# Performance work log

Hardware: AMD Instinct MI355X
Metric: run time of the kernel (lower is better)

Reference implementation:

```python
import jax, jax.numpy as jnp
import numpy as np

B, C, D, O = 64, 64, 512, 256
N_REG, G = 8, 8  # 8 regions of 8 channels


def setup_inputs() -> dict:
    key = jax.random.key(0)
    ks = jax.random.split(key, 9)
    std = 0.02  # init_weights_classify: normal(0, 0.02) for Linear weights, zero bias
    x = jax.random.normal(ks[0], (B, C, D), dtype=jnp.float32)
    region_indices = jnp.arange(C, dtype=jnp.int32).reshape(N_REG, G)
    # attn_fc: Linear(2D -> D), ReLU, Linear(D -> 1)
    W1 = jax.random.normal(ks[1], (2 * D, D), dtype=jnp.float32) * std
    b1 = jnp.zeros((D,), jnp.float32)
    W2 = jax.random.normal(ks[2], (D, 1), dtype=jnp.float32) * std
    b2 = jnp.zeros((1,), jnp.float32)
    # gcn1: Linear(D -> D); gcn2: Linear(D -> O)
    Wg1 = jax.random.normal(ks[3], (D, D), dtype=jnp.float32) * std
    bg1 = jnp.zeros((D,), jnp.float32)
    Wg2 = jax.random.normal(ks[4], (D, O), dtype=jnp.float32) * std
    bg2 = jnp.zeros((O,), jnp.float32)
    return {"x": x, "W1": W1, "b1": b1, "W2": W2, "b2": b2,
            "Wg1": Wg1, "bg1": bg1, "Wg2": Wg2, "bg2": bg2,
            "region_indices": region_indices}


def _leaky_relu02(z):
    return jnp.where(z >= 0, z, 0.2 * z)


def reference(x, W1, b1, W2, b2, Wg1, bg1, Wg2, bg2, region_indices):
    Bb, Cc, Dd = x.shape
    n_reg, g = region_indices.shape
    # channel -> region id; mask[i,j] = same region and i != j
    rid = jnp.zeros((Cc,), jnp.int32).at[region_indices.reshape(-1)].set(
        jnp.repeat(jnp.arange(n_reg, dtype=jnp.int32), g))
    idx = jnp.arange(Cc)
    mask = (rid[:, None] == rid[None, :]) & (idx[:, None] != idx[None, :])  # [C, C]
    # attn_fc on cat(x_i, x_j): split first linear to avoid [B,C,C,2D] concat
    a = x @ W1[:Dd]   # [B, C, D]
    bpart = x @ W1[Dd:]  # [B, C, D]
    h = jax.nn.relu(a[:, :, None, :] + bpart[:, None, :, :] + b1)  # [B, C, C, D]
    scores = jnp.einsum('bijd,do->bij', h, W2) + b2[0]  # [B, C, C]
    scores = jnp.where(mask[None, :, :], scores, -jnp.inf)
    adj = jax.nn.softmax(scores, axis=-1)  # [B, C, C]
    # gcn1: adj @ x -> Linear -> LeakyReLU(0.2); residual mix
    m1 = jnp.einsum('bij,bjd->bid', adj, x)
    x1 = _leaky_relu02(m1 @ Wg1 + bg1)
    x1 = 0.5 * x1 + 0.5 * x
    # gcn2
    m2 = jnp.einsum('bij,bjd->bid', adj, x1)
    out = _leaky_relu02(m2 @ Wg2 + bg2)  # [B, C, O]
    return out
```

## Files before the change

### kernel.cpp

```cpp
#include <hip/hip_runtime.h>
#include <math.h>

#define B_   64
#define C_   64
#define D_   512
#define O_   256
#define NREG 8
#define G_   8
#define M_   (B_ * C_)

typedef __attribute__((ext_vector_type(8))) short s16x8;
typedef __attribute__((ext_vector_type(4))) float f32x4;
typedef unsigned short u16;
typedef unsigned int   u32;

__device__ __forceinline__ float bf2f(u16 u) {
    u32 v = ((u32)u) << 16;
    return __uint_as_float(v);
}
__device__ __forceinline__ u16 f2bf(float f) {
    u32 u = __float_as_uint(f);
    u32 r = (u + 0x7FFFu + ((u >> 16) & 1u)) >> 16;
    return (u16)r;
}

__global__ void rid_kernel(const int* __restrict__ region_indices, int* __restrict__ rid) {
    int t = threadIdx.x;
    int r = t / G_;
    int ch = region_indices[t];
    rid[ch] = r;
}

__global__ __launch_bounds__(256) void f32_to_bf16_vec(const float* __restrict__ in,
                                                       u16* __restrict__ out, int n8) {
    int i = blockIdx.x * blockDim.x + threadIdx.x;
    if (i >= n8) return;
    const float4* p = (const float4*)(in + (size_t)i * 8);
    float4 v0 = p[0], v1 = p[1];
    s16x8 o;
    o[0] = (short)f2bf(v0.x); o[1] = (short)f2bf(v0.y);
    o[2] = (short)f2bf(v0.z); o[3] = (short)f2bf(v0.w);
    o[4] = (short)f2bf(v1.x); o[5] = (short)f2bf(v1.y);
    o[6] = (short)f2bf(v1.z); o[7] = (short)f2bf(v1.w);
    *(s16x8*)(out + (size_t)i * 8) = o;
}

__global__ __launch_bounds__(256) void transpose_to_bf16(const float* __restrict__ W,
                                                         u16* __restrict__ Wt, int K, int N) {
    __shared__ float tile[32][33];
    int n0 = blockIdx.x * 32, k0 = blockIdx.y * 32;
    int tx = threadIdx.x, ty = threadIdx.y;
    #pragma unroll
    for (int j = 0; j < 4; j++)
        tile[ty + j * 8][tx] = W[(size_t)(k0 + ty + j * 8) * N + n0 + tx];
    __syncthreads();
    #pragma unroll
    for (int j = 0; j < 4; j++)
        Wt[(size_t)(n0 + ty + j * 8) * K + k0 + tx] = f2bf(tile[tx][ty + j * 8]);
}

#define LDP 40

template<int BM, int BN, int EPI>
__global__ __launch_bounds__(256)
void mfma_gemm(const u16* __restrict__ A, const u16* __restrict__ Bt, int ldbt,
               u16* __restrict__ Cbf0, u16* __restrict__ Cbf1,
               const float* __restrict__ bias, const float* __restrict__ resid,
               float* __restrict__ Cf)
{
    constexpr int K   = 512;
    constexpr int MR  = BM / 32;
    constexpr int NR  = BN / 32;
    constexpr int CHA = (BM * 32) / (256 * 8);
    constexpr int CHB = (BN * 32) / (256 * 8);
    constexpr int NBH = 512 / BN;

    __shared__ __align__(16) u16 As[BM][LDP];
    __shared__ __align__(16) u16 Bs[BN][LDP];

    const int tid  = threadIdx.x;
    const int lane = tid & 63, w = tid >> 6;
    const int wr = w >> 1, wc = w & 1;
    const int lr = lane & 15, lq = lane >> 4;

    const int bx = blockIdx.x, by = blockIdx.y;
    const int m0 = by * BM;
    int nbase, koff;
    if (EPI == 0) { nbase = (bx % NBH) * BN; koff = (bx / NBH) * 512; }
    else          { nbase = bx * BN;         koff = 0; }

    const int ar = tid >> 2;
    const int ac = (tid & 3) * 8;

    f32x4 acc[MR][NR] = {};
    s16x8 stA[CHA], stB[CHB];

    auto loadG = [&](int kt) {
        #pragma unroll
        for (int ch = 0; ch < CHA; ch++)
            stA[ch] = *(const s16x8*)(A + (size_t)(m0 + ar + ch * 64) * K + kt + ac);
        #pragma unroll
        for (int ch = 0; ch < CHB; ch++)
            stB[ch] = *(const s16x8*)(Bt + (size_t)(nbase + ar + ch * 64) * ldbt + koff + kt + ac);
    };

    loadG(0);
    for (int kt = 0; kt < K; kt += 32) {
        __syncthreads();
        #pragma unroll
        for (int ch = 0; ch < CHA; ch++)
            *(s16x8*)(&As[ar + ch * 64][ac]) = stA[ch];
        #pragma unroll
        for (int ch = 0; ch < CHB; ch++)
            *(s16x8*)(&Bs[ar + ch * 64][ac]) = stB[ch];
        __syncthreads();
        if (kt + 32 < K) loadG(kt + 32);

        s16x8 af[MR], bfr[NR];
        #pragma unroll
        for (int m = 0; m < MR; m++)
            af[m] = *(const s16x8*)(&As[wr * (BM / 2) + m * 16 + lr][lq * 8]);
        #pragma unroll
        for (int n = 0; n < NR; n++)
            bfr[n] = *(const s16x8*)(&Bs[wc * (BN / 2) + n * 16 + lr][lq * 8]);
        #pragma unroll
        for (int m = 0; m < MR; m++)
            #pragma unroll
            for (int n = 0; n < NR; n++)
                acc[m][n] = __builtin_amdgcn_mfma_f32_16x16x32_bf16(af[m], bfr[n], acc[m][n], 0, 0, 0);
    }

    #pragma unroll
    for (int m = 0; m < MR; m++) {
        #pragma unroll
        for (int n = 0; n < NR; n++) {
            #pragma unroll
            for (int j = 0; j < 4; j++) {
                int row = m0 + wr * (BM / 2) + m * 16 + lq * 4 + j;
                int col = nbase + wc * (BN / 2) + n * 16 + lr;
                float v = acc[m][n][j];
                if (EPI == 0) {
                    u16* dst = koff ? Cbf1 : Cbf0;
                    dst[(size_t)row * 512 + col] = f2bf(v);
                } else if (EPI == 1) {
                    v += bias[col];
                    v = (v >= 0.f) ? v : 0.2f * v;
                    v = 0.5f * v + 0.5f * resid[(size_t)row * 512 + col];
                    Cbf0[(size_t)row * 512 + col] = f2bf(v);
                } else {
                    v += bias[col];
                    v = (v >= 0.f) ? v : 0.2f * v;
                    Cf[(size_t)row * 256 + col] = v;
                }
            }
        }
    }
}

__global__ __launch_bounds__(64)
void scores_m1_kernel(const u16* __restrict__ a, const u16* __restrict__ bpart,
                      const float* __restrict__ x,
                      const float* __restrict__ b1, const float* __restrict__ W2,
                      const float* __restrict__ b2,
                      const int* __restrict__ region_indices, const int* __restrict__ rid,
                      float* __restrict__ adjw, u16* __restrict__ m1)
{
    const int lane = threadIdx.x;
    const int bi = blockIdx.x;
    const int b = bi / C_, i = bi % C_;
    const int r = rid[i];

    int members[G_];
    #pragma unroll
    for (int m = 0; m < G_; m++) members[m] = region_indices[r * G_ + m];

    const int d0 = lane * 8;
    float ai[8], w2v[8];
    s16x8 av8 = *(const s16x8*)(a + (size_t)bi * D_ + d0);
    const float4* b1v = (const float4*)(b1 + d0);
    const float4* w2p = (const float4*)(W2 + d0);
    float4 b1a = b1v[0], b1b = b1v[1];
    float4 w2a = w2p[0], w2b = w2p[1];
    ai[0] = bf2f((u16)av8[0]) + b1a.x; ai[1] = bf2f((u16)av8[1]) + b1a.y;
    ai[2] = bf2f((u16)av8[2]) + b1a.z; ai[3] = bf2f((u16)av8[3]) + b1a.w;
    ai[4] = bf2f((u16)av8[4]) + b1b.x; ai[5] = bf2f((u16)av8[5]) + b1b.y;
    ai[6] = bf2f((u16)av8[6]) + b1b.z; ai[7] = bf2f((u16)av8[7]) + b1b.w;
    w2v[0] = w2a.x; w2v[1] = w2a.y; w2v[2] = w2a.z; w2v[3] = w2a.w;
    w2v[4] = w2b.x; w2v[5] = w2b.y; w2v[6] = w2b.z; w2v[7] = w2b.w;

    const float bias2 = b2[0];
    float sc[G_];
    float scmax = -INFINITY;
    for (int m = 0; m < G_; m++) {
        int j = members[m];
        if (j == i) { sc[m] = -INFINITY; continue; }
        s16x8 bv8 = *(const s16x8*)(bpart + ((size_t)(b * C_ + j)) * D_ + d0);
        float p = 0.f;
        #pragma unroll
        for (int t = 0; t < 8; t++) {
            float h = ai[t] + bf2f((u16)bv8[t]);
            h = (h > 0.f) ? h : 0.f;
            p += h * w2v[t];
        }
        #pragma unroll
        for (int off = 32; off >= 1; off >>= 1) p += __shfl_xor(p, off);
        sc[m] = p + bias2;
        scmax = fmaxf(scmax, sc[m]);
    }

    float esum = 0.f, wgt[G_];
    for (int m = 0; m < G_; m++) {
        if (sc[m] == -INFINITY) { wgt[m] = 0.f; continue; }
        wgt[m] = expf(sc[m] - scmax);
        esum += wgt[m];
    }
    const float inv = 1.f / esum;

    float accv[8] = {};
    for (int m = 0; m < G_; m++) {
        wgt[m] *= inv;
        if (wgt[m] == 0.f) continue;
        int j = members[m];
        const float4* xp = (const float4*)(x + ((size_t)(b * C_ + j)) * D_ + d0);
        float4 xa = xp[0], xb = xp[1];
        accv[0] += wgt[m] * xa.x; accv[1] += wgt[m] * xa.y;
        accv[2] += wgt[m] * xa.z; accv[3] += wgt[m] * xa.w;
        accv[4] += wgt[m] * xb.x; accv[5] += wgt[m] * xb.y;
        accv[6] += wgt[m] * xb.z; accv[7] += wgt[m] * xb.w;
    }
    s16x8 o;
    #pragma unroll
    for (int t = 0; t < 8; t++) o[t] = (short)f2bf(accv[t]);
    *(s16x8*)(m1 + (size_t)bi * D_ + d0) = o;

    if (lane < G_) adjw[(size_t)bi * G_ + lane] = wgt[lane];
}

__global__ __launch_bounds__(64)
void m2_kernel(const u16* __restrict__ x1,
               const int* __restrict__ region_indices, const int* __restrict__ rid,
               const float* __restrict__ adjw, u16* __restrict__ m2)
{
    const int lane = threadIdx.x;
    const int bi = blockIdx.x;
    const int b = bi / C_, i = bi % C_;
    const int r = rid[i];
    const int d0 = lane * 8;

    float accv[8] = {};
    for (int m = 0; m < G_; m++) {
        float wm = adjw[(size_t)bi * G_ + m];
        if (wm == 0.f) continue;
        int j = region_indices[r * G_ + m];
        s16x8 v = *(const s16x8*)(x1 + ((size_t)(b * C_ + j)) * D_ + d0);
        #pragma unroll
        for (int t = 0; t < 8; t++) accv[t] += wm * bf2f((u16)v[t]);
    }
    s16x8 o;
    #pragma unroll
    for (int t = 0; t < 8; t++) o[t] = (short)f2bf(accv[t]);
    *(s16x8*)(m2 + (size_t)bi * D_ + d0) = o;
}

extern "C" void kernel_launch(void* const* d_in, const int* in_sizes, int n_in,
                              void* d_out, int out_size, void* d_ws, size_t ws_size,
                              hipStream_t stream) {
    const float* x    = (const float*)d_in[0];
    const float* W1   = (const float*)d_in[1];
    const float* b1   = (const float*)d_in[2];
    const float* W2   = (const float*)d_in[3];
    const float* b2   = (const float*)d_in[4];
    const float* Wg1  = (const float*)d_in[5];
    const float* bg1  = (const float*)d_in[6];
    const float* Wg2  = (const float*)d_in[7];
    const float* bg2  = (const float*)d_in[8];
    const int* region_indices = (const int*)d_in[9];
    float* out = (float*)d_out;

    char* ws = (char*)d_ws;
    const size_t MB = 1024 * 1024;
    u16*   x_bf  = (u16*)(ws);
    u16*   W1t   = (u16*)(ws + 4 * MB);
    u16*   Wg1t  = (u16*)(ws + 5 * MB);
    u16*   Wg2t  = (u16*)(ws + 5 * MB + 512 * 1024);
    u16*   a_bf  = (u16*)(ws + 6 * MB);
    u16*   bp_bf = (u16*)(ws + 10 * MB);
    u16*   m1_bf = (u16*)(ws + 14 * MB);
    u16*   x1_bf = a_bf;
    u16*   m2_bf = bp_bf;
    float* adjw  = (float*)(ws + 18 * MB);
    int*   rid   = (int*)(ws + 18 * MB + 256 * 1024);

    rid_kernel<<<1, 64, 0, stream>>>(region_indices, rid);
    f32_to_bf16_vec<<<(M_ * D_ / 8 + 255) / 256, 256, 0, stream>>>(x, x_bf, M_ * D_ / 8);
    transpose_to_bf16<<<dim3(512 / 32, 1024 / 32), dim3(32, 8), 0, stream>>>(W1,  W1t,  1024, 512);
    transpose_to_bf16<<<dim3(512 / 32, 512 / 32),  dim3(32, 8), 0, stream>>>(Wg1, Wg1t, 512,  512);
    transpose_to_bf16<<<dim3(256 / 32, 512 / 32),  dim3(32, 8), 0, stream>>>(Wg2, Wg2t, 512,  256);

    mfma_gemm<128, 64, 0><<<dim3(16, 32), 256, 0, stream>>>(
        x_bf, W1t, 1024, a_bf, bp_bf, nullptr, nullptr, nullptr);

    scores_m1_kernel<<<M_, 64, 0, stream>>>(a_bf, bp_bf, x, b1, W2, b2,
                                            region_indices, rid, adjw, m1_bf);

    mfma_gemm<64, 64, 1><<<dim3(8, 64), 256, 0, stream>>>(
        m1_bf, Wg1t, 512, x1_bf, nullptr, bg1, x, nullptr);

    m2_kernel<<<M_, 64, 0, stream>>>(x1_bf, region_indices, rid, adjw, m2_bf);

    mfma_gemm<64, 64, 2><<<dim3(4, 64), 256, 0, stream>>>(
        m2_bf, Wg2t, 512, nullptr, nullptr, bg2, nullptr, out);
}
```

Measured before the change: 137.9 us.

## Fuse prep kernels, double-buffer GEMM with direct-to-LDS loads, batch softmax reductions

Merges the five preprocessing launches (x conversion, three weight transposes, region map) into one kernel. Rewrites the MFMA GEMM to use BK=64, double-buffered LDS filled through global_load_lds with an XOR swizzle, so each k-step needs one barrier and register staging goes away. Changes the scores kernel to load all eight neighbour rows up front and interleave the eight wave reductions, and packs four rows per 256-thread block in the scores and m2 kernels. This trades fewer launches and better latency hiding for more LDS per block and tighter correctness requirements on the swizzle and the async loads.

After: 120.5 us. -12.6%, faster.

```diff
diff --git a/kernel.cpp b/kernel.cpp
--- a/kernel.cpp
+++ b/kernel.cpp
@@ -5,129 +5,137 @@
 #define C_   64
 #define D_   512
 #define O_   256
-#define NREG 8
 #define G_   8
-#define M_   (B_ * C_)
+#define M_   4096
 
 typedef __attribute__((ext_vector_type(8))) short s16x8;
 typedef __attribute__((ext_vector_type(4))) float f32x4;
 typedef unsigned short u16;
 typedef unsigned int   u32;
 
-__device__ __forceinline__ float bf2f(u16 u) {
-    u32 v = ((u32)u) << 16;
-    return __uint_as_float(v);
-}
+__device__ __forceinline__ float bf2f(u16 u) { return __uint_as_float(((u32)u) << 16); }
 __device__ __forceinline__ u16 f2bf(float f) {
     u32 u = __float_as_uint(f);
-    u32 r = (u + 0x7FFFu + ((u >> 16) & 1u)) >> 16;
-    return (u16)r;
-}
-
-__global__ void rid_kernel(const int* __restrict__ region_indices, int* __restrict__ rid) {
-    int t = threadIdx.x;
-    int r = t / G_;
-    int ch = region_indices[t];
-    rid[ch] = r;
-}
-
-__global__ __launch_bounds__(256) void f32_to_bf16_vec(const float* __restrict__ in,
-                                                       u16* __restrict__ out, int n8) {
-    int i = blockIdx.x * blockDim.x + threadIdx.x;
-    if (i >= n8) return;
-    const float4* p = (const float4*)(in + (size_t)i * 8);
-    float4 v0 = p[0], v1 = p[1];
-    s16x8 o;
-    o[0] = (short)f2bf(v0.x); o[1] = (short)f2bf(v0.y);
-    o[2] = (short)f2bf(v0.z); o[3] = (short)f2bf(v0.w);
-    o[4] = (short)f2bf(v1.x); o[5] = (short)f2bf(v1.y);
-    o[6] = (short)f2bf(v1.z); o[7] = (short)f2bf(v1.w);
-    *(s16x8*)(out + (size_t)i * 8) = o;
-}
-
-__global__ __launch_bounds__(256) void transpose_to_bf16(const float* __restrict__ W,
-                                                         u16* __restrict__ Wt, int K, int N) {
+    return (u16)((u + 0x7FFFu + ((u >> 16) & 1u)) >> 16);
+}
+__device__ __forceinline__ void gload16(const void* g, void* l) {
+    __builtin_amdgcn_global_load_lds((const __attribute__((address_space(1))) u32*)g,
+                                     (__attribute__((address_space(3))) u32*)l, 16, 0, 0);
+}
+
+__global__ __launch_bounds__(256)
+void prep_kernel(const float* __restrict__ x, u16* __restrict__ x_bf,
+                 const float* __restrict__ W1, u16* __restrict__ W1t,
+                 const float* __restrict__ Wg1, u16* __restrict__ Wg1t,
+                 const float* __restrict__ Wg2, u16* __restrict__ Wg2t,
+                 const int* __restrict__ region_indices, int* __restrict__ rid)
+{
     __shared__ float tile[32][33];
-    int n0 = blockIdx.x * 32, k0 = blockIdx.y * 32;
-    int tx = threadIdx.x, ty = threadIdx.y;
+    const int bx = blockIdx.x, tid = threadIdx.x;
+    if (bx < 1024) {
+        size_t i = ((size_t)bx * 256 + tid) * 8;
+        const float4* p = (const float4*)(x + i);
+        float4 v0 = p[0], v1 = p[1];
+        s16x8 o;
+        o[0] = (short)f2bf(v0.x); o[1] = (short)f2bf(v0.y);
+        o[2] = (short)f2bf(v0.z); o[3] = (short)f2bf(v0.w);
+        o[4] = (short)f2bf(v1.x); o[5] = (short)f2bf(v1.y);
+        o[6] = (short)f2bf(v1.z); o[7] = (short)f2bf(v1.w);
+        *(s16x8*)(x_bf + i) = o;
+        return;
+    }
+    if (bx >= 1920) {
+        if (tid < 64) rid[region_indices[tid]] = tid >> 3;
+        return;
+    }
+    const float* src; u16* dst; int k0, n0, nsrc, obase;
+    if (bx < 1536) {
+        int idx = bx - 1024, h = idx >> 8, t = idx & 255;
+        int tn = t & 15, tk = t >> 4;
+        src = W1 + (size_t)h * 512 * 512; dst = W1t; obase = h * 512;
+        k0 = tk * 32; n0 = tn * 32; nsrc = 512;
+    } else if (bx < 1792) {
+        int t = bx - 1536, tn = t & 15, tk = t >> 4;
+        src = Wg1; dst = Wg1t; obase = 0;
+        k0 = tk * 32; n0 = tn * 32; nsrc = 512;
+    } else {
+        int t = bx - 1792, tn = t & 7, tk = t >> 3;
+        src = Wg2; dst = Wg2t; obase = 0;
+        k0 = tk * 32; n0 = tn * 32; nsrc = 256;
+    }
+    int tx = tid & 31, ty = tid >> 5;
     #pragma unroll
     for (int j = 0; j < 4; j++)
-        tile[ty + j * 8][tx] = W[(size_t)(k0 + ty + j * 8) * N + n0 + tx];
+        tile[ty + j * 8][tx] = src[(size_t)(k0 + ty + j * 8) * nsrc + n0 + tx];
     __syncthreads();
     #pragma unroll
     for (int j = 0; j < 4; j++)
-        Wt[(size_t)(n0 + ty + j * 8) * K + k0 + tx] = f2bf(tile[tx][ty + j * 8]);
-}
-
-#define LDP 40
+        dst[(size_t)(obase + n0 + ty + j * 8) * 512 + k0 + tx] = f2bf(tile[tx][ty + j * 8]);
+}
 
 template<int BM, int BN, int EPI>
 __global__ __launch_bounds__(256)
-void mfma_gemm(const u16* __restrict__ A, const u16* __restrict__ Bt, int ldbt,
-               u16* __restrict__ Cbf0, u16* __restrict__ Cbf1,
+void mfma_gemm(const u16* __restrict__ A, const u16* __restrict__ Bt,
+               u16* __restrict__ Obf0, u16* __restrict__ Obf1,
                const float* __restrict__ bias, const float* __restrict__ resid,
-               float* __restrict__ Cf)
+               float* __restrict__ Of)
 {
-    constexpr int K   = 512;
-    constexpr int MR  = BM / 32;
-    constexpr int NR  = BN / 32;
-    constexpr int CHA = (BM * 32) / (256 * 8);
-    constexpr int CHB = (BN * 32) / (256 * 8);
-    constexpr int NBH = 512 / BN;
-
-    __shared__ __align__(16) u16 As[BM][LDP];
-    __shared__ __align__(16) u16 Bs[BN][LDP];
-
-    const int tid  = threadIdx.x;
-    const int lane = tid & 63, w = tid >> 6;
-    const int wr = w >> 1, wc = w & 1;
+    constexpr int K = 512, BK = 64, NT = K / BK;
+    constexpr int MR = BM / 32, NR = BN / 32;
+    constexpr int CA = BM / 32, CB = BN / 32;
+
+    __shared__ __align__(16) u16 As[2][BM * BK];
+    __shared__ __align__(16) u16 Bs[2][BN * BK];
+
+    const int tid = threadIdx.x;
+    const int lane = tid & 63;
+    const int w = tid >> 6, wr = w >> 1, wc = w & 1;
     const int lr = lane & 15, lq = lane >> 4;
-
-    const int bx = blockIdx.x, by = blockIdx.y;
-    const int m0 = by * BM;
-    int nbase, koff;
-    if (EPI == 0) { nbase = (bx % NBH) * BN; koff = (bx / NBH) * 512; }
-    else          { nbase = bx * BN;         koff = 0; }
-
-    const int ar = tid >> 2;
-    const int ac = (tid & 3) * 8;
+    const int m0 = blockIdx.y * BM, n0 = blockIdx.x * BN;
+
+    const int sr  = tid >> 3;
+    const int ss  = tid & 7;
+    const int gsl = ss ^ (sr & 7);
 
     f32x4 acc[MR][NR] = {};
-    s16x8 stA[CHA], stB[CHB];
-
-    auto loadG = [&](int kt) {
-        #pragma unroll
-        for (int ch = 0; ch < CHA; ch++)
-            stA[ch] = *(const s16x8*)(A + (size_t)(m0 + ar + ch * 64) * K + kt + ac);
-        #pragma unroll
-        for (int ch = 0; ch < CHB; ch++)
-            stB[ch] = *(const s16x8*)(Bt + (size_t)(nbase + ar + ch * 64) * ldbt + koff + kt + ac);
+
+    auto stage = [&](int buf, int kt) {
+        #pragma unroll
+        for (int ch = 0; ch < CA; ch++)
+            gload16(A + (size_t)(m0 + ch * 32 + sr) * K + kt + gsl * 8,
+                    &As[buf][ch * 2048 + tid * 8]);
+        #pragma unroll
+        for (int ch = 0; ch < CB; ch++)
+            gload16(Bt + (size_t)(n0 + ch * 32 + sr) * K + kt + gsl * 8,
+                    &Bs[buf][ch * 2048 + tid * 8]);
     };
 
-    loadG(0);
-    for (int kt = 0; kt < K; kt += 32) {
+    stage(0, 0);
+    int cur = 0;
+    for (int t = 0; t < NT; t++) {
         __syncthreads();
-        #pragma unroll
-        for (int ch = 0; ch < CHA; ch++)
-            *(s16x8*)(&As[ar + ch * 64][ac]) = stA[ch];
-        #pragma unroll
-        for (int ch = 0; ch < CHB; ch++)
-            *(s16x8*)(&Bs[ar + ch * 64][ac]) = stB[ch];
-        __syncthreads();
-        if (kt + 32 < K) loadG(kt + 32);
-
-        s16x8 af[MR], bfr[NR];
-        #pragma unroll
-        for (int m = 0; m < MR; m++)
-            af[m] = *(const s16x8*)(&As[wr * (BM / 2) + m * 16 + lr][lq * 8]);
-        #pragma unroll
-        for (int n = 0; n < NR; n++)
-            bfr[n] = *(const s16x8*)(&Bs[wc * (BN / 2) + n * 16 + lr][lq * 8]);
-        #pragma unroll
-        for (int m = 0; m < MR; m++)
+        if (t + 1 < NT) stage(cur ^ 1, (t + 1) * BK);
+        const u16* as = As[cur]; const u16* bs = Bs[cur];
+        #pragma unroll
+        for (int ks = 0; ks < 2; ks++) {
+            s16x8 af[MR], bfv[NR];
             #pragma unroll
-            for (int n = 0; n < NR; n++)
-                acc[m][n] = __builtin_amdgcn_mfma_f32_16x16x32_bf16(af[m], bfr[n], acc[m][n], 0, 0, 0);
+            for (int m = 0; m < MR; m++) {
+                int r = wr * (BM / 2) + m * 16 + lr;
+                af[m] = *(const s16x8*)(as + r * 64 + (((ks * 4 + lq) ^ (r & 7)) * 8));
+            }
+            #pragma unroll
+            for (int n = 0; n < NR; n++) {
+                int r = wc * (BN / 2) + n * 16 + lr;
+                bfv[n] = *(const s16x8*)(bs + r * 64 + (((ks * 4 + lq) ^ (r & 7)) * 8));
+            }
+            #pragma unroll
+            for (int m = 0; m < MR; m++)
+                #pragma unroll
+                for (int n = 0; n < NR; n++)
+                    acc[m][n] = __builtin_amdgcn_mfma_f32_16x16x32_bf16(af[m], bfv[n], acc[m][n], 0, 0, 0);
+        }
+        cur ^= 1;
     }
 
     #pragma unroll
@@ -137,27 +145,27 @@
             #pragma unroll
             for (int j = 0; j < 4; j++) {
                 int row = m0 + wr * (BM / 2) + m * 16 + lq * 4 + j;
-                int col = nbase + wc * (BN / 2) + n * 16 + lr;
+                int col = n0 + wc * (BN / 2) + n * 16 + lr;
                 float v = acc[m][n][j];
                 if (EPI == 0) {
-                    u16* dst = koff ? Cbf1 : Cbf0;
-                    dst[(size_t)row * 512 + col] = f2bf(v);
+                    if (col < 512) Obf0[(size_t)row * 512 + col] = f2bf(v);
+                    else           Obf1[(size_t)row * 512 + col - 512] = f2bf(v);
                 } else if (EPI == 1) {
                     v += bias[col];
                     v = (v >= 0.f) ? v : 0.2f * v;
                     v = 0.5f * v + 0.5f * resid[(size_t)row * 512 + col];
-                    Cbf0[(size_t)row * 512 + col] = f2bf(v);
+                    Obf0[(size_t)row * 512 + col] = f2bf(v);
                 } else {
                     v += bias[col];
                     v = (v >= 0.f) ? v : 0.2f * v;
-                    Cf[(size_t)row * 256 + col] = v;
+                    Of[(size_t)row * 256 + col] = v;
                 }
             }
         }
     }
 }
 
-__global__ __launch_bounds__(64)
+__global__ __launch_bounds__(256)
 void scores_m1_kernel(const u16* __restrict__ a, const u16* __restrict__ bpart,
                       const float* __restrict__ x,
                       const float* __restrict__ b1, const float* __restrict__ W2,
@@ -165,101 +173,103 @@
                       const int* __restrict__ region_indices, const int* __restrict__ rid,
                       float* __restrict__ adjw, u16* __restrict__ m1)
 {
-    const int lane = threadIdx.x;
-    const int bi = blockIdx.x;
-    const int b = bi / C_, i = bi % C_;
+    const int lane = threadIdx.x & 63;
+    const int bi = blockIdx.x * 4 + (threadIdx.x >> 6);
+    const int b = bi >> 6, i = bi & 63;
     const int r = rid[i];
-
-    int members[G_];
-    #pragma unroll
-    for (int m = 0; m < G_; m++) members[m] = region_indices[r * G_ + m];
+    int members[8];
+    #pragma unroll
+    for (int m = 0; m < 8; m++) members[m] = region_indices[r * 8 + m];
 
     const int d0 = lane * 8;
-    float ai[8], w2v[8];
-    s16x8 av8 = *(const s16x8*)(a + (size_t)bi * D_ + d0);
-    const float4* b1v = (const float4*)(b1 + d0);
-    const float4* w2p = (const float4*)(W2 + d0);
-    float4 b1a = b1v[0], b1b = b1v[1];
-    float4 w2a = w2p[0], w2b = w2p[1];
-    ai[0] = bf2f((u16)av8[0]) + b1a.x; ai[1] = bf2f((u16)av8[1]) + b1a.y;
-    ai[2] = bf2f((u16)av8[2]) + b1a.z; ai[3] = bf2f((u16)av8[3]) + b1a.w;
-    ai[4] = bf2f((u16)av8[4]) + b1b.x; ai[5] = bf2f((u16)av8[5]) + b1b.y;
-    ai[6] = bf2f((u16)av8[6]) + b1b.z; ai[7] = bf2f((u16)av8[7]) + b1b.w;
-    w2v[0] = w2a.x; w2v[1] = w2a.y; w2v[2] = w2a.z; w2v[3] = w2a.w;
-    w2v[4] = w2b.x; w2v[5] = w2b.y; w2v[6] = w2b.z; w2v[7] = w2b.w;
+    s16x8 av8 = *(const s16x8*)(a + (size_t)bi * 512 + d0);
+    float4 b1a = *(const float4*)(b1 + d0), b1b = *(const float4*)(b1 + d0 + 4);
+    float4 w2a = *(const float4*)(W2 + d0), w2b = *(const float4*)(W2 + d0 + 4);
+    float ai[8] = { bf2f((u16)av8[0]) + b1a.x, bf2f((u16)av8[1]) + b1a.y,
+                    bf2f((u16)av8[2]) + b1a.z, bf2f((u16)av8[3]) + b1a.w,
+                    bf2f((u16)av8[4]) + b1b.x, bf2f((u16)av8[5]) + b1b.y,
+                    bf2f((u16)av8[6]) + b1b.z, bf2f((u16)av8[7]) + b1b.w };
+    float w2v[8] = { w2a.x, w2a.y, w2a.z, w2a.w, w2b.x, w2b.y, w2b.z, w2b.w };
+
+    s16x8 bv[8];
+    #pragma unroll
+    for (int m = 0; m < 8; m++)
+        bv[m] = *(const s16x8*)(bpart + ((size_t)(b * 64 + members[m])) * 512 + d0);
+
+    float p[8];
+    #pragma unroll
+    for (int m = 0; m < 8; m++) {
+        float s = 0.f;
+        #pragma unroll
+        for (int t = 0; t < 8; t++) {
+            float h = ai[t] + bf2f((u16)bv[m][t]);
+            s += fmaxf(h, 0.f) * w2v[t];
+        }
+        p[m] = s;
+    }
+    #pragma unroll
+    for (int off = 32; off >= 1; off >>= 1)
+        #pragma unroll
+        for (int m = 0; m < 8; m++) p[m] += __shfl_xor(p[m], off);
 
     const float bias2 = b2[0];
-    float sc[G_];
     float scmax = -INFINITY;
-    for (int m = 0; m < G_; m++) {
-        int j = members[m];
-        if (j == i) { sc[m] = -INFINITY; continue; }
-        s16x8 bv8 = *(const s16x8*)(bpart + ((size_t)(b * C_ + j)) * D_ + d0);
-        float p = 0.f;
-        #pragma unroll
-        for (int t = 0; t < 8; t++) {
-            float h = ai[t] + bf2f((u16)bv8[t]);
-            h = (h > 0.f) ? h : 0.f;
-            p += h * w2v[t];
+    #pragma unroll
+    for (int m = 0; m < 8; m++) {
+        p[m] = (members[m] == i) ? -INFINITY : p[m] + bias2;
+        scmax = fmaxf(scmax, p[m]);
+    }
+    float esum = 0.f;
+    #pragma unroll
+    for (int m = 0; m < 8; m++) {
+        p[m] = (members[m] == i) ? 0.f : __expf(p[m] - scmax);
+        esum += p[m];
+    }
+    const float inv = 1.f / esum;
+
+    float accv[8] = {};
+    #pragma unroll
+    for (int m = 0; m < 8; m++) {
+        p[m] *= inv;
+        if (members[m] != i) {
+            const float4* xp = (const float4*)(x + ((size_t)(b * 64 + members[m])) * 512 + d0);
+            float4 xa = xp[0], xb = xp[1];
+            accv[0] += p[m] * xa.x; accv[1] += p[m] * xa.y;
+            accv[2] += p[m] * xa.z; accv[3] += p[m] * xa.w;
+            accv[4] += p[m] * xb.x; accv[5] += p[m] * xb.y;
+            accv[6] += p[m] * xb.z; accv[7] += p[m] * xb.w;
         }
-        #pragma unroll
-        for (int off = 32; off >= 1; off >>= 1) p += __shfl_xor(p, off);
-        sc[m] = p + bias2;
-        scmax = fmaxf(scmax, sc[m]);
-    }
-
-    float esum = 0.f, wgt[G_];
-    for (int m = 0; m < G_; m++) {
-        if (sc[m] == -INFINITY) { wgt[m] = 0.f; continue; }
-        wgt[m] = expf(sc[m] - scmax);
-        esum += wgt[m];
-    }
-    const float inv = 1.f / esum;
-
-    float accv[8] = {};
-    for (int m = 0; m < G_; m++) {
-        wgt[m] *= inv;
-        if (wgt[m] == 0.f) continue;
-        int j = members[m];
-        const float4* xp = (const float4*)(x + ((size_t)(b * C_ + j)) * D_ + d0);
-        float4 xa = xp[0], xb = xp[1];
-        accv[0] += wgt[m] * xa.x; accv[1] += wgt[m] * xa.y;
-        accv[2] += wgt[m] * xa.z; accv[3] += wgt[m] * xa.w;
-        accv[4] += wgt[m] * xb.x; accv[5] += wgt[m] * xb.y;
-        accv[6] += wgt[m] * xb.z; accv[7] += wgt[m] * xb.w;
     }
     s16x8 o;
     #pragma unroll
     for (int t = 0; t < 8; t++) o[t] = (short)f2bf(accv[t]);
-    *(s16x8*)(m1 + (size_t)bi * D_ + d0) = o;
-
-    if (lane < G_) adjw[(size_t)bi * G_ + lane] = wgt[lane];
-}
-
-__global__ __launch_bounds__(64)
+    *(s16x8*)(m1 + (size_t)bi * 512 + d0) = o;
+    if (lane < 8) adjw[(size_t)bi * 8 + lane] = p[lane];
+}
+
+__global__ __launch_bounds__(256)
 void m2_kernel(const u16* __restrict__ x1,
                const int* __restrict__ region_indices, const int* __restrict__ rid,
                const float* __restrict__ adjw, u16* __restrict__ m2)
 {
-    const int lane = threadIdx.x;
-    const int bi = blockIdx.x;
-    const int b = bi / C_, i = bi % C_;
+    const int lane = threadIdx.x & 63;
+    const int bi = blockIdx.x * 4 + (threadIdx.x >> 6);
+    const int b = bi >> 6, i = bi & 63;
     const int r = rid[i];
     const int d0 = lane * 8;
-
     float accv[8] = {};
-    for (int m = 0; m < G_; m++) {
-        float wm = adjw[(size_t)bi * G_ + m];
-        if (wm == 0.f) continue;
-        int j = region_indices[r * G_ + m];
-        s16x8 v = *(const s16x8*)(x1 + ((size_t)(b * C_ + j)) * D_ + d0);
+    #pragma unroll
+    for (int m = 0; m < 8; m++) {
+        float wm = adjw[(size_t)bi * 8 + m];
+        int j = region_indices[r * 8 + m];
+        s16x8 v = *(const s16x8*)(x1 + ((size_t)(b * 64 + j)) * 512 + d0);
         #pragma unroll
         for (int t = 0; t < 8; t++) accv[t] += wm * bf2f((u16)v[t]);
     }
     s16x8 o;
     #pragma unroll
     for (int t = 0; t < 8; t++) o[t] = (short)f2bf(accv[t]);
-    *(s16x8*)(m2 + (size_t)bi * D_ + d0) = o;
+    *(s16x8*)(m2 + (size_t)bi * 512 + d0) = o;
 }
 
 extern "C" void kernel_launch(void* const* d_in, const int* in_sizes, int n_in,
@@ -291,23 +301,20 @@
     float* adjw  = (float*)(ws + 18 * MB);
     int*   rid   = (int*)(ws + 18 * MB + 256 * 1024);
 
-    rid_kernel<<<1, 64, 0, stream>>>(region_indices, rid);
-    f32_to_bf16_vec<<<(M_ * D_ / 8 + 255) / 256, 256, 0, stream>>>(x, x_bf, M_ * D_ / 8);
-    transpose_to_bf16<<<dim3(512 / 32, 1024 / 32), dim3(32, 8), 0, stream>>>(W1,  W1t,  1024, 512);
-    transpose_to_bf16<<<dim3(512 / 32, 512 / 32),  dim3(32, 8), 0, stream>>>(Wg1, Wg1t, 512,  512);
-    transpose_to_bf16<<<dim3(256 / 32, 512 / 32),  dim3(32, 8), 0, stream>>>(Wg2, Wg2t, 512,  256);
+    prep_kernel<<<1921, 256, 0, stream>>>(x, x_bf, W1, W1t, Wg1, Wg1t, Wg2, Wg2t,
+                                          region_indices, rid);
 
     mfma_gemm<128, 64, 0><<<dim3(16, 32), 256, 0, stream>>>(
-        x_bf, W1t, 1024, a_bf, bp_bf, nullptr, nullptr, nullptr);
-
-    scores_m1_kernel<<<M_, 64, 0, stream>>>(a_bf, bp_bf, x, b1, W2, b2,
-                                            region_indices, rid, adjw, m1_bf);
+        x_bf, W1t, a_bf, bp_bf, nullptr, nullptr, nullptr);
+
+    scores_m1_kernel<<<1024, 256, 0, stream>>>(a_bf, bp_bf, x, b1, W2, b2,
+                                               region_indices, rid, adjw, m1_bf);
 
     mfma_gemm<64, 64, 1><<<dim3(8, 64), 256, 0, stream>>>(
-        m1_bf, Wg1t, 512, x1_bf, nullptr, bg1, x, nullptr);
-
-    m2_kernel<<<M_, 64, 0, stream>>>(x1_bf, region_indices, rid, adjw, m2_bf);
+        m1_bf, Wg1t, x1_bf, nullptr, bg1, x, nullptr);
+
+    m2_kernel<<<1024, 256, 0, stream>>>(x1_bf, region_indices, rid, adjw, m2_bf);
 
     mfma_gemm<64, 64, 2><<<dim3(4, 64), 256, 0, stream>>>(
-        m2_bf, Wg2t, 512, nullptr, nullptr, bg2, nullptr, out);
-}
+        m2_bf, Wg2t, nullptr, nullptr, bg2, nullptr, out);
+}
```
